# Performance work log

Measured on AMD Instinct MI355X. Metric: run time of the kernel, lower is better.

The kernel has to match this reference:

```python
import jax, jax.numpy as jnp
import numpy as np

N_NODES = 100000
IN_CH = 128
HID = 16
N_EDGES = 3200000


def setup_inputs() -> dict:
    key = jax.random.key(0)
    k1, k2, k3, k4 = jax.random.split(key, 4)
    x = jax.random.normal(k1, (N_NODES, IN_CH), dtype=jnp.float32)
    edge_index = jax.random.randint(k2, (2, N_EDGES), 0, N_NODES, dtype=jnp.int64)
    s1 = 1.0 / np.sqrt(IN_CH)
    s2 = 1.0 / np.sqrt(HID)
    W1 = jax.random.uniform(k3, (IN_CH, HID), dtype=jnp.float32, minval=-s1, maxval=s1)
    b1 = jnp.zeros((HID,), dtype=jnp.float32)
    W2 = jax.random.uniform(k4, (HID, HID), dtype=jnp.float32, minval=-s2, maxval=s2)
    b2 = jnp.zeros((HID,), dtype=jnp.float32)
    return {"x": x, "edge_index": edge_index, "W1": W1, "b1": b1, "W2": W2, "b2": b2}


def _gcn_layer(h, W, b, row, col, norm, n_nodes):
    # GCNConv: transform first (small hidden dim), then normalized sum aggregation
    h = h @ W  # [N, out]
    msg = h[row] * norm[:, None]  # gather over edges incl. self-loops
    out = jax.ops.segment_sum(msg, col, num_segments=n_nodes)
    return out + b


def reference(x, edge_index, W1, b1, W2, b2):
    n = x.shape[0]
    row, col = edge_index[0], edge_index[1]
    # add self-loops (PyG GCNConv default)
    loop = jnp.arange(n, dtype=edge_index.dtype)
    row_l = jnp.concatenate([row, loop])
    col_l = jnp.concatenate([col, loop])
    # symmetric normalization D^-1/2 (A+I) D^-1/2 (degree from target index)
    deg = jax.ops.segment_sum(jnp.ones_like(col_l, dtype=x.dtype), col_l, num_segments=n)
    dinv = jnp.where(deg > 0, jax.lax.rsqrt(deg), 0.0)
    norm = dinv[row_l] * dinv[col_l]

    h = _gcn_layer(x, W1, b1, row_l, col_l, norm, n)
    h = jax.nn.relu(h)  # dropout is identity at eval
    h = _gcn_layer(h, W2, b2, row_l, col_l, norm, n)

    # fused per-edge dot-product link score + sigmoid (original edges only)
    scores = jnp.sum(h[row] * h[col], axis=-1)
    return jax.nn.sigmoid(scores)
```

## Files before the change

kernel.cpp:

```cpp
#include <hip/hip_runtime.h>
#include <hip/hip_bf16.h>
#include <hip/hip_fp16.h>
#include <math.h>


#define BSH 7
#define BSZ 128
#define CAPB 8192
#define RCAP 12
#define MAXCH 3200
#define MAXCHUNKS 1024

__global__ __launch_bounds__(1024) void pSort(
    const int* __restrict__ row, const int* __restrict__ col,
    int* __restrict__ gcur, unsigned int* __restrict__ ebuf,
    int E, int CH, int NBUK) {
    __shared__ unsigned int se[MAXCH];
    __shared__ unsigned short pk[MAXCH];
    __shared__ int lhist[1024], lbase[1024], lcur[1024], gbase[1024];
    const int t = threadIdx.x, b = blockIdx.x;
    lhist[t] = 0;
    __syncthreads();
    const int s = b * CH, e = min(E, s + CH);
    const int cnt = e - s;
    const int n4 = cnt >> 2;
    const int4* c4 = (const int4*)(col + s);
    const int4* r4 = (const int4*)(row + s);
    for (int i = t; i < n4; i += 1024) {
        int4 c = c4[i];
        atomicAdd(&lhist[c.x >> BSH], 1);
        atomicAdd(&lhist[c.y >> BSH], 1);
        atomicAdd(&lhist[c.z >> BSH], 1);
        atomicAdd(&lhist[c.w >> BSH], 1);
    }
    for (int i = (n4 << 2) + t; i < cnt; i += 1024) atomicAdd(&lhist[col[s + i] >> BSH], 1);
    __syncthreads();
    {
        int own = lhist[t];
        lcur[t] = own;
        __syncthreads();
        for (int d = 1; d < 1024; d <<= 1) {
            int add = (t >= d) ? lcur[t - d] : 0;
            __syncthreads();
            lcur[t] += add;
            __syncthreads();
        }
        lbase[t] = lcur[t] - own;
        lcur[t] = lbase[t];
        __syncthreads();
        if (t < NBUK) {
            int base = atomicAdd(&gcur[t], lhist[t]);
            gbase[t] = t * CAPB + base - lbase[t];
        }
    }
    __syncthreads();
    for (int i = t; i < n4; i += 1024) {
        int4 c = c4[i];
        int4 r = r4[i];
        int k0 = c.x >> BSH, p0 = atomicAdd(&lcur[k0], 1);
        se[p0] = ((unsigned int)(c.x & (BSZ - 1)) << 17) | (unsigned int)r.x; pk[p0] = (unsigned short)k0;
        int k1 = c.y >> BSH, p1 = atomicAdd(&lcur[k1], 1);
        se[p1] = ((unsigned int)(c.y & (BSZ - 1)) << 17) | (unsigned int)r.y; pk[p1] = (unsigned short)k1;
        int k2 = c.z >> BSH, p2 = atomicAdd(&lcur[k2], 1);
        se[p2] = ((unsigned int)(c.z & (BSZ - 1)) << 17) | (unsigned int)r.z; pk[p2] = (unsigned short)k2;
        int k3 = c.w >> BSH, p3 = atomicAdd(&lcur[k3], 1);
        se[p3] = ((unsigned int)(c.w & (BSZ - 1)) << 17) | (unsigned int)r.w; pk[p3] = (unsigned short)k3;
    }
    for (int i = (n4 << 2) + t; i < cnt; i += 1024) {
        int c = col[s + i], r = row[s + i];
        int k = c >> BSH, p = atomicAdd(&lcur[k], 1);
        se[p] = ((unsigned int)(c & (BSZ - 1)) << 17) | (unsigned int)r; pk[p] = (unsigned short)k;
    }
    __syncthreads();
    for (int i = t; i < cnt; i += 1024) {
        int k = pk[i];
        ebuf[gbase[k] + i] = se[i];
    }
}

__global__ __launch_bounds__(512) void pS2G(
    const unsigned int* __restrict__ ebuf, const int* __restrict__ gcur,
    const float* __restrict__ x, const float* __restrict__ W1,
    unsigned int* __restrict__ ebuf2, float* __restrict__ dinv,
    int* __restrict__ start, __half* __restrict__ ts, int N) {
    __shared__ int h[BSZ], sc[BSZ], cur[BSZ];
    __shared__ float wsT[16 * 132];
    const int t = threadIdx.x, k = blockIdx.x;
    if (t < BSZ) h[t] = 0;
    for (int idx = t; idx < 2048; idx += 512) {
        int kk = idx >> 4, c = idx & 15;
        wsT[c * 132 + kk] = W1[idx];
    }
    __syncthreads();
    const int s = k * CAPB, e = s + gcur[k];
    const int cnt = e - s;
    unsigned int r[RCAP];
    const bool fits = (cnt <= 512 * RCAP);
    if (fits) {
        int nr = 0;
        for (int i = s + t; i < e; i += 512) {
            unsigned int w = ebuf[i];
            r[nr++] = w;
            atomicAdd(&h[w >> 17], 1);
        }
    } else {
        for (int i = s + t; i < e; i += 512) atomicAdd(&h[ebuf[i] >> 17], 1);
    }
    __syncthreads();
    if (t < BSZ) sc[t] = h[t];
    __syncthreads();
    for (int d = 1; d < BSZ; d <<= 1) {
        int add = (t < BSZ && t >= d) ? sc[t - d] : 0;
        __syncthreads();
        if (t < BSZ) sc[t] += add;
        __syncthreads();
    }
    if (t < BSZ) {
        cur[t] = sc[t] - h[t];
        const int v = (k << BSH) + t;
        if (v < N) {
            dinv[v] = rsqrtf((float)h[t] + 1.0f);
            start[v] = s + cur[t];
        }
    }
    __syncthreads();
    if (fits) {
        int nr = 0;
        for (int i = s + t; i < e; i += 512) {
            unsigned int w = r[nr++];
            int p = atomicAdd(&cur[w >> 17], 1);
            ebuf2[s + p] = w;
        }
    } else {
        for (int i = s + t; i < e; i += 512) {
            unsigned int w = ebuf[i];
            int p = atomicAdd(&cur[w >> 17], 1);
            ebuf2[s + p] = w;
        }
    }
    const int u = t >> 2, q = t & 3;
    const int v = (k << BSH) + u;
    if (v >= N) return;
    const float dv = rsqrtf((float)h[u] + 1.0f);
    const float4* xr = (const float4*)(x + (size_t)v * 128);
    float acc[16];
    #pragma unroll
    for (int c = 0; c < 16; ++c) acc[c] = 0.f;
    #pragma unroll
    for (int k4 = 0; k4 < 8; ++k4) {
        const int kk = q + 4 * k4;
        float4 a = xr[kk];
        #pragma unroll
        for (int c = 0; c < 16; ++c) {
            const float4 w = *(const float4*)&wsT[c * 132 + kk * 4];
            acc[c] = fmaf(a.x, w.x, fmaf(a.y, w.y, fmaf(a.z, w.z, fmaf(a.w, w.w, acc[c]))));
        }
    }
    #pragma unroll
    for (int c = 0; c < 16; ++c) {
        acc[c] += __shfl_xor(acc[c], 1);
        acc[c] += __shfl_xor(acc[c], 2);
    }
    union { __half h4[4]; uint2 u2; } o;
    #pragma unroll
    for (int c = 0; c < 4; ++c) o.h4[c] = __float2half(acc[q * 4 + c] * dv);
    ((uint2*)(ts + (size_t)v * 16))[q] = o.u2;
}

__global__ __launch_bounds__(256) void pGat1(
    const unsigned int* __restrict__ ebuf2, const int* __restrict__ start,
    const int* __restrict__ gcur,
    const __half2* __restrict__ tsv, const float* __restrict__ dinv,
    const float* __restrict__ b1, const float* __restrict__ W2,
    __half2* __restrict__ ts2v, int N) {
    __shared__ float w2s[256];
    const int tid = threadIdx.x;
    w2s[tid] = W2[tid];
    __syncthreads();
    const int l = tid & 7;
    const int v = blockIdx.x * 32 + (tid >> 3);
    if (v >= N) return;
    const int s = start[v];
    const int k = v >> BSH;
    const bool lastv = (((v + 1) & (BSZ - 1)) == 0) || (v + 1 >= N);
    const int e = lastv ? (k * CAPB + gcur[k]) : start[v + 1];
    float sx = 0.f, sy = 0.f;
    int i = s;
    for (; i + 8 <= e; i += 8) {
        unsigned int w0 = ebuf2[i],     w1 = ebuf2[i + 1];
        unsigned int w2 = ebuf2[i + 2], w3 = ebuf2[i + 3];
        unsigned int w4 = ebuf2[i + 4], w5 = ebuf2[i + 5];
        unsigned int w6 = ebuf2[i + 6], w7 = ebuf2[i + 7];
        float2 f0 = __half22float2(tsv[(size_t)(w0 & 0x1FFFF) * 8 + l]);
        float2 f1 = __half22float2(tsv[(size_t)(w1 & 0x1FFFF) * 8 + l]);
        float2 f2 = __half22float2(tsv[(size_t)(w2 & 0x1FFFF) * 8 + l]);
        float2 f3 = __half22float2(tsv[(size_t)(w3 & 0x1FFFF) * 8 + l]);
        float2 f4 = __half22float2(tsv[(size_t)(w4 & 0x1FFFF) * 8 + l]);
        float2 f5 = __half22float2(tsv[(size_t)(w5 & 0x1FFFF) * 8 + l]);
        float2 f6 = __half22float2(tsv[(size_t)(w6 & 0x1FFFF) * 8 + l]);
        float2 f7 = __half22float2(tsv[(size_t)(w7 & 0x1FFFF) * 8 + l]);
        sx += ((f0.x + f1.x) + (f2.x + f3.x)) + ((f4.x + f5.x) + (f6.x + f7.x));
        sy += ((f0.y + f1.y) + (f2.y + f3.y)) + ((f4.y + f5.y) + (f6.y + f7.y));
    }
    for (; i + 4 <= e; i += 4) {
        unsigned int w0 = ebuf2[i],     w1 = ebuf2[i + 1];
        unsigned int w2 = ebuf2[i + 2], w3 = ebuf2[i + 3];
        float2 f0 = __half22float2(tsv[(size_t)(w0 & 0x1FFFF) * 8 + l]);
        float2 f1 = __half22float2(tsv[(size_t)(w1 & 0x1FFFF) * 8 + l]);
        float2 f2 = __half22float2(tsv[(size_t)(w2 & 0x1FFFF) * 8 + l]);
        float2 f3 = __half22float2(tsv[(size_t)(w3 & 0x1FFFF) * 8 + l]);
        sx += (f0.x + f1.x) + (f2.x + f3.x);
        sy += (f0.y + f1.y) + (f2.y + f3.y);
    }
    for (; i < e; ++i) {
        unsigned int w = ebuf2[i];
        float2 f = __half22float2(tsv[(size_t)(w & 0x1FFFF) * 8 + l]);
        sx += f.x; sy += f.y;
    }
    const float dv = dinv[v];
    float2 sf = __half22float2(tsv[(size_t)v * 8 + l]);
    float hx = fmaxf(dv * (sx + sf.x) + b1[2 * l],     0.f);
    float hy = fmaxf(dv * (sy + sf.y) + b1[2 * l + 1], 0.f);
    float ox = 0.f, oy = 0.f;
    #pragma unroll
    for (int j = 0; j < 8; ++j) {
        float ax = __shfl(hx, j, 8);
        float ay = __shfl(hy, j, 8);
        ox = fmaf(ax, w2s[(2 * j) * 16 + 2 * l],     fmaf(ay, w2s[(2 * j + 1) * 16 + 2 * l],     ox));
        oy = fmaf(ax, w2s[(2 * j) * 16 + 2 * l + 1], fmaf(ay, w2s[(2 * j + 1) * 16 + 2 * l + 1], oy));
    }
    ts2v[(size_t)v * 8 + l] = __halves2half2(__float2half(dv * ox), __float2half(dv * oy));
}

__global__ __launch_bounds__(256) void pGat2(
    const unsigned int* __restrict__ ebuf2, const int* __restrict__ start,
    const int* __restrict__ gcur,
    const __half2* __restrict__ tsv, const float* __restrict__ dinv,
    const float* __restrict__ b2, __half2* __restrict__ h2v, int N) {
    const int tid = threadIdx.x;
    const int l = tid & 7;
    const int v = blockIdx.x * 32 + (tid >> 3);
    if (v >= N) return;
    const int s = start[v];
    const int k = v >> BSH;
    const bool lastv = (((v + 1) & (BSZ - 1)) == 0) || (v + 1 >= N);
    const int e = lastv ? (k * CAPB + gcur[k]) : start[v + 1];
    float sx = 0.f, sy = 0.f;
    int i = s;
    for (; i + 8 <= e; i += 8) {
        unsigned int w0 = ebuf2[i],     w1 = ebuf2[i + 1];
        unsigned int w2 = ebuf2[i + 2], w3 = ebuf2[i + 3];
        unsigned int w4 = ebuf2[i + 4], w5 = ebuf2[i + 5];
        unsigned int w6 = ebuf2[i + 6], w7 = ebuf2[i + 7];
        float2 f0 = __half22float2(tsv[(size_t)(w0 & 0x1FFFF) * 8 + l]);
        float2 f1 = __half22float2(tsv[(size_t)(w1 & 0x1FFFF) * 8 + l]);
        float2 f2 = __half22float2(tsv[(size_t)(w2 & 0x1FFFF) * 8 + l]);
        float2 f3 = __half22float2(tsv[(size_t)(w3 & 0x1FFFF) * 8 + l]);
        float2 f4 = __half22float2(tsv[(size_t)(w4 & 0x1FFFF) * 8 + l]);
        float2 f5 = __half22float2(tsv[(size_t)(w5 & 0x1FFFF) * 8 + l]);
        float2 f6 = __half22float2(tsv[(size_t)(w6 & 0x1FFFF) * 8 + l]);
        float2 f7 = __half22float2(tsv[(size_t)(w7 & 0x1FFFF) * 8 + l]);
        sx += ((f0.x + f1.x) + (f2.x + f3.x)) + ((f4.x + f5.x) + (f6.x + f7.x));
        sy += ((f0.y + f1.y) + (f2.y + f3.y)) + ((f4.y + f5.y) + (f6.y + f7.y));
    }
    for (; i + 4 <= e; i += 4) {
        unsigned int w0 = ebuf2[i],     w1 = ebuf2[i + 1];
        unsigned int w2 = ebuf2[i + 2], w3 = ebuf2[i + 3];
        float2 f0 = __half22float2(tsv[(size_t)(w0 & 0x1FFFF) * 8 + l]);
        float2 f1 = __half22float2(tsv[(size_t)(w1 & 0x1FFFF) * 8 + l]);
        float2 f2 = __half22float2(tsv[(size_t)(w2 & 0x1FFFF) * 8 + l]);
        float2 f3 = __half22float2(tsv[(size_t)(w3 & 0x1FFFF) * 8 + l]);
        sx += (f0.x + f1.x) + (f2.x + f3.x);
        sy += (f0.y + f1.y) + (f2.y + f3.y);
    }
    for (; i < e; ++i) {
        unsigned int w = ebuf2[i];
        float2 f = __half22float2(tsv[(size_t)(w & 0x1FFFF) * 8 + l]);
        sx += f.x; sy += f.y;
    }
    float2 sf = __half22float2(tsv[(size_t)v * 8 + l]);
    const float dv = dinv[v];
    h2v[(size_t)v * 8 + l] = __halves2half2(
        __float2half(dv * (sx + sf.x) + b2[2 * l]),
        __float2half(dv * (sy + sf.y) + b2[2 * l + 1]));
}

__global__ void k_score(const int* __restrict__ row, const int* __restrict__ col,
                        const __half* __restrict__ h2h, float* __restrict__ out, int E) {
    int e = blockIdx.x * 256 + threadIdx.x;
    if (e < E) {
        union { uint4 u[2]; __half2 h[8]; } a, b;
        const uint4* pa = (const uint4*)(h2h + (size_t)row[e] * 16);
        const uint4* pb = (const uint4*)(h2h + (size_t)col[e] * 16);
        a.u[0] = pa[0]; a.u[1] = pa[1];
        b.u[0] = pb[0]; b.u[1] = pb[1];
        float d = 0.f;
        #pragma unroll
        for (int i = 0; i < 8; ++i) {
            float2 fa = __half22float2(a.h[i]);
            float2 fb = __half22float2(b.h[i]);
            d = fmaf(fa.x, fb.x, fmaf(fa.y, fb.y, d));
        }
        out[e] = 1.0f / (1.0f + __expf(-d));
    }
}

__global__ void k_countf(const int* __restrict__ col, float* __restrict__ deg, int E) {
    int e = blockIdx.x * 256 + threadIdx.x;
    if (e < E) atomicAdd(&deg[col[e]], 1.0f);
}
__global__ void k_dinvf(float* __restrict__ dinv, int N) {
    int v = blockIdx.x * 256 + threadIdx.x;
    if (v < N) dinv[v] = rsqrtf(dinv[v] + 1.0f);
}
__global__ __launch_bounds__(256) void k_gemm1f(
    const float* __restrict__ x, const float* __restrict__ W1,
    const float* __restrict__ dinv, float* __restrict__ ts, int N) {
    __shared__ float wsT[16 * 132];
    const int tid = threadIdx.x;
    for (int idx = tid; idx < 2048; idx += 256) {
        int k = idx >> 4, c = idx & 15;
        wsT[c * 132 + k] = W1[idx];
    }
    __syncthreads();
    const int n = blockIdx.x * 256 + tid;
    if (n >= N) return;
    const float4* xr = (const float4*)(x + (size_t)n * 128);
    float acc[16];
    #pragma unroll
    for (int c = 0; c < 16; ++c) acc[c] = 0.f;
    for (int k4 = 0; k4 < 32; ++k4) {
        float4 a = xr[k4];
        #pragma unroll
        for (int c = 0; c < 16; ++c) {
            const float4 w = *(const float4*)&wsT[c * 132 + k4 * 4];
            acc[c] = fmaf(a.x, w.x, fmaf(a.y, w.y, fmaf(a.z, w.z, fmaf(a.w, w.w, acc[c]))));
        }
    }
    float dv = dinv[n];
    float4* o = (float4*)(ts + (size_t)n * 16);
    #pragma unroll
    for (int q = 0; q < 4; ++q)
        o[q] = make_float4(acc[4*q] * dv, acc[4*q+1] * dv, acc[4*q+2] * dv, acc[4*q+3] * dv);
}
__global__ void k_scatter(const int* __restrict__ row, const int* __restrict__ col,
                          const float* __restrict__ ts, float* __restrict__ acc, int E) {
    int g = blockIdx.x * 256 + threadIdx.x;
    int e = g >> 4, c = g & 15;
    if (e < E) atomicAdd(&acc[(size_t)col[e] * 16 + c], ts[(size_t)row[e] * 16 + c]);
}
__global__ void k_finalize(float* __restrict__ acc, const float* __restrict__ ts,
                           const float* __restrict__ dinv, const float* __restrict__ b,
                           int N, int relu) {
    int g = blockIdx.x * 256 + threadIdx.x;
    int v = g >> 4, c = g & 15;
    if (v < N) {
        float h = dinv[v] * (acc[g] + ts[g]) + b[c];
        if (relu) h = fmaxf(h, 0.f);
        acc[g] = h;
    }
}
__global__ __launch_bounds__(256) void k_gemm2f(
    const float* __restrict__ h1, const float* __restrict__ W2,
    const float* __restrict__ dinv, float* __restrict__ ts2, int N) {
    __shared__ float hs[16 * 17];
    __shared__ float ws2[256];
    const int tid = threadIdx.x;
    const int base = blockIdx.x * 16;
    if (tid < 64) ((float4*)ws2)[tid] = ((const float4*)W2)[tid];
    if (tid >= 64 && tid < 128) {
        int t2 = tid - 64;
        float4 v4 = ((const float4*)(h1 + (size_t)base * 16))[t2];
        float* d = &hs[(t2 >> 2) * 17 + (t2 & 3) * 4];
        d[0] = v4.x; d[1] = v4.y; d[2] = v4.z; d[3] = v4.w;
    }
    __syncthreads();
    const int r = tid >> 4, c = tid & 15;
    float a = 0.f;
    #pragma unroll
    for (int kk = 0; kk < 16; ++kk) a = fmaf(hs[r * 17 + kk], ws2[kk * 16 + c], a);
    ts2[(size_t)(base + r) * 16 + c] = a * dinv[base + r];
}
__global__ void k_scoref(const int* __restrict__ row, const int* __restrict__ col,
                         const float* __restrict__ h2, float* __restrict__ out, int E) {
    int e = blockIdx.x * 256 + threadIdx.x;
    if (e < E) {
        const float4* a = (const float4*)(h2 + (size_t)row[e] * 16);
        const float4* b = (const float4*)(h2 + (size_t)col[e] * 16);
        float d = 0.f;
        #pragma unroll
        for (int i = 0; i < 4; ++i) {
            float4 u = a[i], v = b[i];
            d += u.x * v.x + u.y * v.y + u.z * v.z + u.w * v.w;
        }
        out[e] = 1.0f / (1.0f + __expf(-d));
    }
}

extern "C" void kernel_launch(void* const* d_in, const int* in_sizes, int n_in,
                              void* d_out, int out_size, void* d_ws, size_t ws_size,
                              hipStream_t stream) {
    const float* x  = (const float*)d_in[0];
    const int*   ei = (const int*)d_in[1];
    const float* W1 = (const float*)d_in[2];
    const float* b1 = (const float*)d_in[3];
    const float* W2 = (const float*)d_in[4];
    const float* b2 = (const float*)d_in[5];

    const int N = in_sizes[0] / 128;
    const int E = in_sizes[1] / 2;
    const int* row = ei;
    const int* col = ei + E;
    float* out = (float*)d_out;

    const int NBUK = (N + BSZ - 1) / BSZ;
    const int CN = (E + MAXCH - 1) / MAXCH;
    const int CH = MAXCH;

    char* ws = (char*)d_ws;
    size_t off = 0;
    auto alloc = [&](size_t bytes) { void* p = ws + off; off += (bytes + 255) & ~(size_t)255; return p; };
    float*  dinv  = (float*)alloc((size_t)N * 4);
    __half* ts1h  = (__half*)alloc((size_t)N * 32);
    __half* ts2h  = (__half*)alloc((size_t)N * 32);
    int*    start = (int*)alloc((size_t)(N + 1) * 4);
    int*    gcur  = (int*)alloc((size_t)NBUK * 4);
    unsigned int* ebuf  = (unsigned int*)alloc((size_t)NBUK * CAPB * 4);
    unsigned int* ebuf2 = (unsigned int*)alloc((size_t)NBUK * CAPB * 4);
    const size_t need = off;

    if (N <= 131072 && NBUK <= 1024 && CN <= MAXCHUNKS &&
        (size_t)E * 2 <= (size_t)NBUK * CAPB && ws_size >= need) {
        hipMemsetAsync(gcur, 0, (size_t)NBUK * 4, stream);
        pSort<<<CN, 1024, 0, stream>>>(row, col, gcur, ebuf, E, CH, NBUK);
        pS2G<<<NBUK, 512, 0, stream>>>(ebuf, gcur, x, W1, ebuf2, dinv, start, ts1h, N);
        pGat1<<<(N + 31) / 32, 256, 0, stream>>>(ebuf2, start, gcur, (const __half2*)ts1h,
                                                 dinv, b1, W2, (__half2*)ts2h, N);
        __half* h2h = ts1h;
        pGat2<<<(N + 31) / 32, 256, 0, stream>>>(ebuf2, start, gcur, (const __half2*)ts2h,
                                                 dinv, b2, (__half2*)h2h, N);
        k_score<<<(E + 255) / 256, 256, 0, stream>>>(row, col, h2h, out, E);
    } else {
        float* dinvF = (float*)ws;
        float* ts1F  = (float*)(ws + (size_t)N * 4);
        float* ts2F  = (float*)(ws + (size_t)N * 4 + (size_t)N * 64);
        hipMemsetAsync(dinvF, 0, (size_t)N * 4, stream);
        hipMemsetAsync(ts2F, 0, (size_t)N * 64, stream);
        k_countf<<<(E + 255) / 256, 256, 0, stream>>>(col, dinvF, E);
        k_dinvf<<<(N + 255) / 256, 256, 0, stream>>>(dinvF, N);
        k_gemm1f<<<(N + 255) / 256, 256, 0, stream>>>(x, W1, dinvF, ts1F, N);
        k_scatter<<<(E * 16) / 256, 256, 0, stream>>>(row, col, ts1F, ts2F, E);
        k_finalize<<<(N * 16 + 255) / 256, 256, 0, stream>>>(ts2F, ts1F, dinvF, b1, N, 1);
        k_gemm2f<<<N / 16, 256, 0, stream>>>(ts2F, W2, dinvF, ts1F, N);
        hipMemsetAsync(ts2F, 0, (size_t)N * 64, stream);
        k_scatter<<<(E * 16) / 256, 256, 0, stream>>>(row, col, ts1F, ts2F, E);
        k_finalize<<<(N * 16 + 255) / 256, 256, 0, stream>>>(ts2F, ts1F, dinvF, b2, N, 0);
        k_scoref<<<(E + 255) / 256, 256, 0, stream>>>(row, col, ts2F, out, E);
    }
}
```

Before: 256.6 us.

## Move X·W1 GEMM into sort kernel and widen gather to 16-byte loads

The dense x·W1 transform now runs in extra blocks of the sort kernel, so it overlaps with the edge bucketing, and writes unscaled fp16 rows. pS2G then only rescales each row by its dinv in place. The two gather kernels now use 2 threads per node, each loading 16 bytes (8 halves) per neighbour with deeper unrolling, instead of 8 threads with 4-byte loads. This cuts the number of memory transactions per edge, at the cost of more registers, less parallelism per node and an extra read-modify-write pass over ts1.

```diff
diff --git a/kernel.cpp b/kernel.cpp
--- a/kernel.cpp
+++ b/kernel.cpp
@@ -11,14 +11,46 @@
 #define MAXCH 3200
 #define MAXCHUNKS 1024
 
-__global__ __launch_bounds__(1024) void pSort(
+__global__ __launch_bounds__(1024) void pSortG(
     const int* __restrict__ row, const int* __restrict__ col,
     int* __restrict__ gcur, unsigned int* __restrict__ ebuf,
-    int E, int CH, int NBUK) {
+    const float* __restrict__ x, const float* __restrict__ W1,
+    __half* __restrict__ ts, int E, int CH, int NBUK, int N, int CN) {
     __shared__ unsigned int se[MAXCH];
     __shared__ unsigned short pk[MAXCH];
     __shared__ int lhist[1024], lbase[1024], lcur[1024], gbase[1024];
-    const int t = threadIdx.x, b = blockIdx.x;
+    __shared__ float wsT[16 * 132];
+    const int t = threadIdx.x;
+    if (blockIdx.x >= CN) {
+        const int b = blockIdx.x - CN;
+        for (int idx = t; idx < 2048; idx += 1024) {
+            int kk = idx >> 4, c = idx & 15;
+            wsT[c * 132 + kk] = W1[idx];
+        }
+        __syncthreads();
+        const int n = b * 1024 + t;
+        if (n >= N) return;
+        const float4* xr = (const float4*)(x + (size_t)n * 128);
+        float acc[16];
+        #pragma unroll
+        for (int c = 0; c < 16; ++c) acc[c] = 0.f;
+        #pragma unroll 4
+        for (int k4 = 0; k4 < 32; ++k4) {
+            float4 a = xr[k4];
+            #pragma unroll
+            for (int c = 0; c < 16; ++c) {
+                const float4 w = *(const float4*)&wsT[c * 132 + k4 * 4];
+                acc[c] = fmaf(a.x, w.x, fmaf(a.y, w.y, fmaf(a.z, w.z, fmaf(a.w, w.w, acc[c]))));
+            }
+        }
+        union { __half h[16]; uint4 u[2]; } o;
+        #pragma unroll
+        for (int c = 0; c < 16; ++c) o.h[c] = __float2half(acc[c]);
+        uint4* dst = (uint4*)(ts + (size_t)n * 16);
+        dst[0] = o.u[0]; dst[1] = o.u[1];
+        return;
+    }
+    const int b = blockIdx.x;
     lhist[t] = 0;
     __syncthreads();
     const int s = b * CH, e = min(E, s + CH);
@@ -80,17 +112,11 @@
 
 __global__ __launch_bounds__(512) void pS2G(
     const unsigned int* __restrict__ ebuf, const int* __restrict__ gcur,
-    const float* __restrict__ x, const float* __restrict__ W1,
     unsigned int* __restrict__ ebuf2, float* __restrict__ dinv,
     int* __restrict__ start, __half* __restrict__ ts, int N) {
     __shared__ int h[BSZ], sc[BSZ], cur[BSZ];
-    __shared__ float wsT[16 * 132];
     const int t = threadIdx.x, k = blockIdx.x;
     if (t < BSZ) h[t] = 0;
-    for (int idx = t; idx < 2048; idx += 512) {
-        int kk = idx >> 4, c = idx & 15;
-        wsT[c * 132 + kk] = W1[idx];
-    }
     __syncthreads();
     const int s = k * CAPB, e = s + gcur[k];
     const int cnt = e - s;
@@ -142,147 +168,160 @@
     const int v = (k << BSH) + u;
     if (v >= N) return;
     const float dv = rsqrtf((float)h[u] + 1.0f);
-    const float4* xr = (const float4*)(x + (size_t)v * 128);
-    float acc[16];
-    #pragma unroll
-    for (int c = 0; c < 16; ++c) acc[c] = 0.f;
-    #pragma unroll
-    for (int k4 = 0; k4 < 8; ++k4) {
-        const int kk = q + 4 * k4;
-        float4 a = xr[kk];
-        #pragma unroll
-        for (int c = 0; c < 16; ++c) {
-            const float4 w = *(const float4*)&wsT[c * 132 + kk * 4];
-            acc[c] = fmaf(a.x, w.x, fmaf(a.y, w.y, fmaf(a.z, w.z, fmaf(a.w, w.w, acc[c]))));
-        }
-    }
-    #pragma unroll
-    for (int c = 0; c < 16; ++c) {
-        acc[c] += __shfl_xor(acc[c], 1);
-        acc[c] += __shfl_xor(acc[c], 2);
-    }
-    union { __half h4[4]; uint2 u2; } o;
-    #pragma unroll
-    for (int c = 0; c < 4; ++c) o.h4[c] = __float2half(acc[q * 4 + c] * dv);
-    ((uint2*)(ts + (size_t)v * 16))[q] = o.u2;
-}
-
-__global__ __launch_bounds__(256) void pGat1(
+    uint2* p2 = (uint2*)(ts + (size_t)v * 16) + q;
+    uint2 w2 = *p2;
+    __half2 a = *(__half2*)&w2.x, b = *(__half2*)&w2.y;
+    float2 fa = __half22float2(a), fb = __half22float2(b);
+    *(__half2*)&w2.x = __floats2half2_rn(fa.x * dv, fa.y * dv);
+    *(__half2*)&w2.y = __floats2half2_rn(fb.x * dv, fb.y * dv);
+    *p2 = w2;
+}
+
+#define ACC8(qq) do {                                        \
+    float2 f_;                                               \
+    f_ = __half22float2(*(const __half2*)&(qq).x); a0 += f_.x; a1 += f_.y; \
+    f_ = __half22float2(*(const __half2*)&(qq).y); a2 += f_.x; a3 += f_.y; \
+    f_ = __half22float2(*(const __half2*)&(qq).z); a4 += f_.x; a5 += f_.y; \
+    f_ = __half22float2(*(const __half2*)&(qq).w); a6 += f_.x; a7 += f_.y; \
+} while (0)
+
+#define GLD(j) tsq[((size_t)(ebuf2[i + (j)] & 0x1FFFF) << 1) + p]
+
+__global__ __launch_bounds__(512) void pGat1(
     const unsigned int* __restrict__ ebuf2, const int* __restrict__ start,
     const int* __restrict__ gcur,
-    const __half2* __restrict__ tsv, const float* __restrict__ dinv,
+    const uint4* __restrict__ tsq, const float* __restrict__ dinv,
     const float* __restrict__ b1, const float* __restrict__ W2,
-    __half2* __restrict__ ts2v, int N) {
+    uint4* __restrict__ ts2q, int N) {
     __shared__ float w2s[256];
     const int tid = threadIdx.x;
-    w2s[tid] = W2[tid];
-    __syncthreads();
-    const int l = tid & 7;
-    const int v = blockIdx.x * 32 + (tid >> 3);
+    if (tid < 256) w2s[tid] = W2[tid];
+    __syncthreads();
+    const int p = tid & 1;
+    const int v = blockIdx.x * 256 + (tid >> 1);
     if (v >= N) return;
     const int s = start[v];
     const int k = v >> BSH;
     const bool lastv = (((v + 1) & (BSZ - 1)) == 0) || (v + 1 >= N);
     const int e = lastv ? (k * CAPB + gcur[k]) : start[v + 1];
-    float sx = 0.f, sy = 0.f;
+    float a0 = 0.f, a1 = 0.f, a2 = 0.f, a3 = 0.f, a4 = 0.f, a5 = 0.f, a6 = 0.f, a7 = 0.f;
     int i = s;
+    for (; i + 16 <= e; i += 16) {
+        uint4 q0 = GLD(0),  q1 = GLD(1),  q2 = GLD(2),  q3 = GLD(3);
+        uint4 q4 = GLD(4),  q5 = GLD(5),  q6 = GLD(6),  q7 = GLD(7);
+        uint4 q8 = GLD(8),  q9 = GLD(9),  qa = GLD(10), qb = GLD(11);
+        uint4 qc = GLD(12), qd = GLD(13), qe = GLD(14), qf = GLD(15);
+        ACC8(q0); ACC8(q1); ACC8(q2); ACC8(q3);
+        ACC8(q4); ACC8(q5); ACC8(q6); ACC8(q7);
+        ACC8(q8); ACC8(q9); ACC8(qa); ACC8(qb);
+        ACC8(qc); ACC8(qd); ACC8(qe); ACC8(qf);
+    }
     for (; i + 8 <= e; i += 8) {
-        unsigned int w0 = ebuf2[i],     w1 = ebuf2[i + 1];
-        unsigned int w2 = ebuf2[i + 2], w3 = ebuf2[i + 3];
-        unsigned int w4 = ebuf2[i + 4], w5 = ebuf2[i + 5];
-        unsigned int w6 = ebuf2[i + 6], w7 = ebuf2[i + 7];
-        float2 f0 = __half22float2(tsv[(size_t)(w0 & 0x1FFFF) * 8 + l]);
-        float2 f1 = __half22float2(tsv[(size_t)(w1 & 0x1FFFF) * 8 + l]);
-        float2 f2 = __half22float2(tsv[(size_t)(w2 & 0x1FFFF) * 8 + l]);
-        float2 f3 = __half22float2(tsv[(size_t)(w3 & 0x1FFFF) * 8 + l]);
-        float2 f4 = __half22float2(tsv[(size_t)(w4 & 0x1FFFF) * 8 + l]);
-        float2 f5 = __half22float2(tsv[(size_t)(w5 & 0x1FFFF) * 8 + l]);
-        float2 f6 = __half22float2(tsv[(size_t)(w6 & 0x1FFFF) * 8 + l]);
-        float2 f7 = __half22float2(tsv[(size_t)(w7 & 0x1FFFF) * 8 + l]);
-        sx += ((f0.x + f1.x) + (f2.x + f3.x)) + ((f4.x + f5.x) + (f6.x + f7.x));
-        sy += ((f0.y + f1.y) + (f2.y + f3.y)) + ((f4.y + f5.y) + (f6.y + f7.y));
+        uint4 q0 = GLD(0), q1 = GLD(1), q2 = GLD(2), q3 = GLD(3);
+        uint4 q4 = GLD(4), q5 = GLD(5), q6 = GLD(6), q7 = GLD(7);
+        ACC8(q0); ACC8(q1); ACC8(q2); ACC8(q3);
+        ACC8(q4); ACC8(q5); ACC8(q6); ACC8(q7);
     }
     for (; i + 4 <= e; i += 4) {
-        unsigned int w0 = ebuf2[i],     w1 = ebuf2[i + 1];
-        unsigned int w2 = ebuf2[i + 2], w3 = ebuf2[i + 3];
-        float2 f0 = __half22float2(tsv[(size_t)(w0 & 0x1FFFF) * 8 + l]);
-        float2 f1 = __half22float2(tsv[(size_t)(w1 & 0x1FFFF) * 8 + l]);
-        float2 f2 = __half22float2(tsv[(size_t)(w2 & 0x1FFFF) * 8 + l]);
-        float2 f3 = __half22float2(tsv[(size_t)(w3 & 0x1FFFF) * 8 + l]);
-        sx += (f0.x + f1.x) + (f2.x + f3.x);
-        sy += (f0.y + f1.y) + (f2.y + f3.y);
+        uint4 q0 = GLD(0), q1 = GLD(1), q2 = GLD(2), q3 = GLD(3);
+        ACC8(q0); ACC8(q1); ACC8(q2); ACC8(q3);
     }
     for (; i < e; ++i) {
-        unsigned int w = ebuf2[i];
-        float2 f = __half22float2(tsv[(size_t)(w & 0x1FFFF) * 8 + l]);
-        sx += f.x; sy += f.y;
+        uint4 q0 = GLD(0);
+        ACC8(q0);
+    }
+    {
+        uint4 sq = tsq[((size_t)v << 1) + p];
+        ACC8(sq);
     }
     const float dv = dinv[v];
-    float2 sf = __half22float2(tsv[(size_t)v * 8 + l]);
-    float hx = fmaxf(dv * (sx + sf.x) + b1[2 * l],     0.f);
-    float hy = fmaxf(dv * (sy + sf.y) + b1[2 * l + 1], 0.f);
-    float ox = 0.f, oy = 0.f;
+    const float4 bA = ((const float4*)b1)[2 * p];
+    const float4 bB = ((const float4*)b1)[2 * p + 1];
+    float h[8];
+    h[0] = fmaxf(fmaf(dv, a0, bA.x), 0.f);
+    h[1] = fmaxf(fmaf(dv, a1, bA.y), 0.f);
+    h[2] = fmaxf(fmaf(dv, a2, bA.z), 0.f);
+    h[3] = fmaxf(fmaf(dv, a3, bA.w), 0.f);
+    h[4] = fmaxf(fmaf(dv, a4, bB.x), 0.f);
+    h[5] = fmaxf(fmaf(dv, a5, bB.y), 0.f);
+    h[6] = fmaxf(fmaf(dv, a6, bB.z), 0.f);
+    h[7] = fmaxf(fmaf(dv, a7, bB.w), 0.f);
+    const int my = p * 8, ot = (1 - p) * 8;
+    float o[8];
+    #pragma unroll
+    for (int c = 0; c < 8; ++c) o[c] = 0.f;
     #pragma unroll
     for (int j = 0; j < 8; ++j) {
-        float ax = __shfl(hx, j, 8);
-        float ay = __shfl(hy, j, 8);
-        ox = fmaf(ax, w2s[(2 * j) * 16 + 2 * l],     fmaf(ay, w2s[(2 * j + 1) * 16 + 2 * l],     ox));
-        oy = fmaf(ax, w2s[(2 * j) * 16 + 2 * l + 1], fmaf(ay, w2s[(2 * j + 1) * 16 + 2 * l + 1], oy));
-    }
-    ts2v[(size_t)v * 8 + l] = __halves2half2(__float2half(dv * ox), __float2half(dv * oy));
-}
-
-__global__ __launch_bounds__(256) void pGat2(
+        float hm = h[j];
+        float ho = __shfl_xor(h[j], 1);
+        #pragma unroll
+        for (int c = 0; c < 8; ++c) {
+            o[c] = fmaf(hm, w2s[(my + j) * 16 + my + c],
+                   fmaf(ho, w2s[(ot + j) * 16 + my + c], o[c]));
+        }
+    }
+    union { __half hh[8]; uint4 u; } ov;
+    #pragma unroll
+    for (int c = 0; c < 8; ++c) ov.hh[c] = __float2half(dv * o[c]);
+    ts2q[((size_t)v << 1) + p] = ov.u;
+}
+
+__global__ __launch_bounds__(512) void pGat2(
     const unsigned int* __restrict__ ebuf2, const int* __restrict__ start,
     const int* __restrict__ gcur,
-    const __half2* __restrict__ tsv, const float* __restrict__ dinv,
-    const float* __restrict__ b2, __half2* __restrict__ h2v, int N) {
+    const uint4* __restrict__ tsq, const float* __restrict__ dinv,
+    const float* __restrict__ b2, uint4* __restrict__ h2q, int N) {
     const int tid = threadIdx.x;
-    const int l = tid & 7;
-    const int v = blockIdx.x * 32 + (tid >> 3);
+    const int p = tid & 1;
+    const int v = blockIdx.x * 256 + (tid >> 1);
     if (v >= N) return;
     const int s = start[v];
     const int k = v >> BSH;
     const bool lastv = (((v + 1) & (BSZ - 1)) == 0) || (v + 1 >= N);
     const int e = lastv ? (k * CAPB + gcur[k]) : start[v + 1];
-    float sx = 0.f, sy = 0.f;
+    float a0 = 0.f, a1 = 0.f, a2 = 0.f, a3 = 0.f, a4 = 0.f, a5 = 0.f, a6 = 0.f, a7 = 0.f;
     int i = s;
+    for (; i + 16 <= e; i += 16) {
+        uint4 q0 = GLD(0),  q1 = GLD(1),  q2 = GLD(2),  q3 = GLD(3);
+        uint4 q4 = GLD(4),  q5 = GLD(5),  q6 = GLD(6),  q7 = GLD(7);
+        uint4 q8 = GLD(8),  q9 = GLD(9),  qa = GLD(10), qb = GLD(11);
+        uint4 qc = GLD(12), qd = GLD(13), qe = GLD(14), qf = GLD(15);
+        ACC8(q0); ACC8(q1); ACC8(q2); ACC8(q3);
+        ACC8(q4); ACC8(q5); ACC8(q6); ACC8(q7);
+        ACC8(q8); ACC8(q9); ACC8(qa); ACC8(qb);
+        ACC8(qc); ACC8(qd); ACC8(qe); ACC8(qf);
+    }
     for (; i + 8 <= e; i += 8) {
-        unsigned int w0 = ebuf2[i],     w1 = ebuf2[i + 1];
-        unsigned int w2 = ebuf2[i + 2], w3 = ebuf2[i + 3];
-        unsigned int w4 = ebuf2[i + 4], w5 = ebuf2[i + 5];
-        unsigned int w6 = ebuf2[i + 6], w7 = ebuf2[i + 7];
-        float2 f0 = __half22float2(tsv[(size_t)(w0 & 0x1FFFF) * 8 + l]);
-        float2 f1 = __half22float2(tsv[(size_t)(w1 & 0x1FFFF) * 8 + l]);
-        float2 f2 = __half22float2(tsv[(size_t)(w2 & 0x1FFFF) * 8 + l]);
-        float2 f3 = __half22float2(tsv[(size_t)(w3 & 0x1FFFF) * 8 + l]);
-        float2 f4 = __half22float2(tsv[(size_t)(w4 & 0x1FFFF) * 8 + l]);
-        float2 f5 = __half22float2(tsv[(size_t)(w5 & 0x1FFFF) * 8 + l]);
-        float2 f6 = __half22float2(tsv[(size_t)(w6 & 0x1FFFF) * 8 + l]);
-        float2 f7 = __half22float2(tsv[(size_t)(w7 & 0x1FFFF) * 8 + l]);
-        sx += ((f0.x + f1.x) + (f2.x + f3.x)) + ((f4.x + f5.x) + (f6.x + f7.x));
-        sy += ((f0.y + f1.y) + (f2.y + f3.y)) + ((f4.y + f5.y) + (f6.y + f7.y));
+        uint4 q0 = GLD(0), q1 = GLD(1), q2 = GLD(2), q3 = GLD(3);
+        uint4 q4 = GLD(4), q5 = GLD(5), q6 = GLD(6), q7 = GLD(7);
+        ACC8(q0); ACC8(q1); ACC8(q2); ACC8(q3);
+        ACC8(q4); ACC8(q5); ACC8(q6); ACC8(q7);
     }
     for (; i + 4 <= e; i += 4) {
-        unsigned int w0 = ebuf2[i],     w1 = ebuf2[i + 1];
-        unsigned int w2 = ebuf2[i + 2], w3 = ebuf2[i + 3];
-        float2 f0 = __half22float2(tsv[(size_t)(w0 & 0x1FFFF) * 8 + l]);
-        float2 f1 = __half22float2(tsv[(size_t)(w1 & 0x1FFFF) * 8 + l]);
-        float2 f2 = __half22float2(tsv[(size_t)(w2 & 0x1FFFF) * 8 + l]);
-        float2 f3 = __half22float2(tsv[(size_t)(w3 & 0x1FFFF) * 8 + l]);
-        sx += (f0.x + f1.x) + (f2.x + f3.x);
-        sy += (f0.y + f1.y) + (f2.y + f3.y);
+        uint4 q0 = GLD(0), q1 = GLD(1), q2 = GLD(2), q3 = GLD(3);
+        ACC8(q0); ACC8(q1); ACC8(q2); ACC8(q3);
     }
     for (; i < e; ++i) {
-        unsigned int w = ebuf2[i];
-        float2 f = __half22float2(tsv[(size_t)(w & 0x1FFFF) * 8 + l]);
-        sx += f.x; sy += f.y;
-    }
-    float2 sf = __half22float2(tsv[(size_t)v * 8 + l]);
+        uint4 q0 = GLD(0);
+        ACC8(q0);
+    }
+    {
+        uint4 sq = tsq[((size_t)v << 1) + p];
+        ACC8(sq);
+    }
     const float dv = dinv[v];
-    h2v[(size_t)v * 8 + l] = __halves2half2(
-        __float2half(dv * (sx + sf.x) + b2[2 * l]),
-        __float2half(dv * (sy + sf.y) + b2[2 * l + 1]));
+    const float4 bA = ((const float4*)b2)[2 * p];
+    const float4 bB = ((const float4*)b2)[2 * p + 1];
+    union { __half hh[8]; uint4 u; } ov;
+    ov.hh[0] = __float2half(fmaf(dv, a0, bA.x));
+    ov.hh[1] = __float2half(fmaf(dv, a1, bA.y));
+    ov.hh[2] = __float2half(fmaf(dv, a2, bA.z));
+    ov.hh[3] = __float2half(fmaf(dv, a3, bA.w));
+    ov.hh[4] = __float2half(fmaf(dv, a4, bB.x));
+    ov.hh[5] = __float2half(fmaf(dv, a5, bB.y));
+    ov.hh[6] = __float2half(fmaf(dv, a6, bB.z));
+    ov.hh[7] = __float2half(fmaf(dv, a7, bB.w));
+    h2q[((size_t)v << 1) + p] = ov.u;
 }
 
 __global__ void k_score(const int* __restrict__ row, const int* __restrict__ col,
@@ -416,6 +455,7 @@
     const int NBUK = (N + BSZ - 1) / BSZ;
     const int CN = (E + MAXCH - 1) / MAXCH;
     const int CH = MAXCH;
+    const int GB = (N + 1023) / 1024;
 
     char* ws = (char*)d_ws;
     size_t off = 0;
@@ -432,13 +472,14 @@
     if (N <= 131072 && NBUK <= 1024 && CN <= MAXCHUNKS &&
         (size_t)E * 2 <= (size_t)NBUK * CAPB && ws_size >= need) {
         hipMemsetAsync(gcur, 0, (size_t)NBUK * 4, stream);
-        pSort<<<CN, 1024, 0, stream>>>(row, col, gcur, ebuf, E, CH, NBUK);
-        pS2G<<<NBUK, 512, 0, stream>>>(ebuf, gcur, x, W1, ebuf2, dinv, start, ts1h, N);
-        pGat1<<<(N + 31) / 32, 256, 0, stream>>>(ebuf2, start, gcur, (const __half2*)ts1h,
-                                                 dinv, b1, W2, (__half2*)ts2h, N);
+        pSortG<<<CN + GB, 1024, 0, stream>>>(row, col, gcur, ebuf, x, W1, ts1h,
+                                             E, CH, NBUK, N, CN);
+        pS2G<<<NBUK, 512, 0, stream>>>(ebuf, gcur, ebuf2, dinv, start, ts1h, N);
+        pGat1<<<(N + 255) / 256, 512, 0, stream>>>(ebuf2, start, gcur, (const uint4*)ts1h,
+                                                   dinv, b1, W2, (uint4*)ts2h, N);
         __half* h2h = ts1h;
-        pGat2<<<(N + 31) / 32, 256, 0, stream>>>(ebuf2, start, gcur, (const __half2*)ts2h,
-                                                 dinv, b2, (__half2*)h2h, N);
+        pGat2<<<(N + 255) / 256, 512, 0, stream>>>(ebuf2, start, gcur, (const uint4*)ts2h,
+                                                   dinv, b2, (uint4*)h2h, N);
         k_score<<<(E + 255) / 256, 256, 0, stream>>>(row, col, h2h, out, E);
     } else {
         float* dinvF = (float*)ws;
```

New measurement: 273.8 us. +6.7%, slower.
